# Performance work log

Measured on AMD Instinct MI355X. Metric: run time of the kernel, lower is better.

## Reference

```python
import jax, jax.numpy as jnp
import numpy as np

N = 100000
E = 3200000
NFEAT = 512
NHID = 256


def setup_inputs() -> dict:
    key = jax.random.key(0)
    ks = jax.random.split(key, 8)
    x = jax.random.normal(ks[0], (N, NFEAT), dtype=jnp.float32)
    edge_row = jax.random.randint(ks[1], (E,), 0, N, dtype=jnp.int32)
    edge_col = jax.random.randint(ks[2], (E,), 0, N, dtype=jnp.int32)
    edge_val = jax.random.uniform(ks[3], (E,), dtype=jnp.float32)
    # xavier_uniform init as in reset_parameters
    lim1 = np.sqrt(6.0 / (NFEAT + NHID)).astype(np.float32)
    lim2 = np.sqrt(6.0 / (NHID + NHID)).astype(np.float32)
    W1 = jax.random.uniform(ks[4], (NFEAT, NHID), minval=-lim1, maxval=lim1, dtype=jnp.float32)
    W2 = jax.random.uniform(ks[5], (NHID, NHID), minval=-lim2, maxval=lim2, dtype=jnp.float32)
    b1 = jnp.zeros((NHID,), dtype=jnp.float32)
    b2 = jnp.zeros((NHID,), dtype=jnp.float32)
    alpha = jnp.full((1,), 0.25, dtype=jnp.float32)  # PReLU single weight
    return {"x": x, "edge_row": edge_row, "edge_col": edge_col,
            "edge_val": edge_val, "W1": W1, "b1": b1, "W2": W2, "b2": b2,
            "alpha": alpha}


def _spmm(edge_row, edge_col, edge_val, support):
    # out[i] = sum over edges e with row[e]==i of val[e] * support[col[e]]
    msgs = support[edge_col] * edge_val[:, None]  # [E, F]
    return jax.ops.segment_sum(msgs, edge_row, num_segments=N)


def _prelu(x, alpha):
    return jnp.where(x >= 0, x, alpha * x)


def reference(x, edge_row, edge_col, edge_val, W1, b1, W2, b2, alpha):
    # Layer 1: GraphConvolution(nfeat, nhid) -> PReLU (dropout=0 -> identity)
    h = _spmm(edge_row, edge_col, edge_val, x @ W1) + b1
    h = _prelu(h, alpha)
    # Layer 2: GraphConvolution(nhid, nhid) -> PReLU
    h = _spmm(edge_row, edge_col, edge_val, h @ W2) + b2
    h = _prelu(h, alpha)
    return h
```

## Files before the change

### kernel.cpp

```cpp
#include <hip/hip_runtime.h>

#define NHID 256
#define BSHIFT 6
#define BROWS  (1 << BSHIFT)
#define MAXNB  1568

typedef __attribute__((ext_vector_type(8))) short short8;
typedef __attribute__((ext_vector_type(4))) float floatx4;
typedef __attribute__((ext_vector_type(4))) float float4v;
typedef __attribute__((ext_vector_type(4))) int int4v;
typedef __attribute__((ext_vector_type(4))) unsigned int uint4v;

static __device__ __forceinline__ short f2bf(float f) {
    unsigned u = __float_as_uint(f);
    unsigned r = (u + 0x7fffu + ((u >> 16) & 1u)) >> 16;
    return (short)r;
}
static __device__ __forceinline__ unsigned pk2(float a, float b) {
    return ((unsigned)(unsigned short)f2bf(a)) | (((unsigned)(unsigned short)f2bf(b)) << 16);
}

__global__ void transpose_cast2(const float* __restrict__ W1, short* __restrict__ W1t,
                                const float* __restrict__ W2, short* __restrict__ W2t,
                                int K1, int K2)
{
    int idx = blockIdx.x * 256 + threadIdx.x;
    int n1 = K1 * NHID;
    if (idx < n1) {
        int k = idx >> 8;
        int n = idx & 255;
        W1t[(size_t)n * K1 + k] = f2bf(W1[idx]);
    } else {
        int j = idx - n1;
        if (j < K2 * NHID) {
            int k = j >> 8;
            int n = j & 255;
            W2t[(size_t)n * K2 + k] = f2bf(W2[j]);
        }
    }
}

template<bool ABF16>
__global__ __launch_bounds__(512) void gemm_mfma(
    const void* __restrict__ Ap, const short* __restrict__ Bt,
    short* __restrict__ C, int M, int K)
{
    __shared__ __align__(16) short As[128][40];
    __shared__ __align__(16) short Bs[256][40];

    int tid  = threadIdx.x;
    int m0   = blockIdx.x * 128;
    int lane = tid & 63;
    int wid  = tid >> 6;
    int wm   = wid >> 2;
    int wn   = wid & 3;
    int quad = lane >> 4;
    int l16  = lane & 15;

    floatx4 acc[4][4] = {};

    for (int k0 = 0; k0 < K; k0 += 32) {
        if (ABF16) {
            const short* A = (const short*)Ap;
            int tr = tid >> 2, tc = (tid & 3) * 8;
            int gm = m0 + tr;
            int4v v = {0, 0, 0, 0};
            if (gm < M) v = __builtin_nontemporal_load((const int4v*)(A + (size_t)gm * K + k0 + tc));
            *(int4v*)&As[tr][tc] = v;
        } else {
            const float* A = (const float*)Ap;
            int tr = tid >> 3, tc = (tid & 7) * 4;
            #pragma unroll
            for (int p = 0; p < 2; ++p) {
                int m = p * 64 + tr, gm = m0 + m;
                float4v v = {0.f, 0.f, 0.f, 0.f};
                if (gm < M) v = __builtin_nontemporal_load((const float4v*)(A + (size_t)gm * K + k0 + tc));
                short4 s;
                s.x = f2bf(v.x); s.y = f2bf(v.y); s.z = f2bf(v.z); s.w = f2bf(v.w);
                *(short4*)&As[m][tc] = s;
            }
        }
        {
            int nr = tid >> 2, nc = (tid & 3) * 8;
            #pragma unroll
            for (int p = 0; p < 2; ++p) {
                int n = p * 128 + nr;
                *(int4*)&Bs[n][nc] = *(const int4*)(Bt + (size_t)n * K + k0 + nc);
            }
        }
        __syncthreads();

        short8 af[4], bfr[4];
        #pragma unroll
        for (int t = 0; t < 4; ++t) {
            af[t]  = *(const short8*)&As[wm * 64 + t * 16 + l16][quad * 8];
            bfr[t] = *(const short8*)&Bs[wn * 64 + t * 16 + l16][quad * 8];
        }
        #pragma unroll
        for (int tm = 0; tm < 4; ++tm)
            #pragma unroll
            for (int tn = 0; tn < 4; ++tn)
                acc[tm][tn] = __builtin_amdgcn_mfma_f32_16x16x32_bf16(
                    af[tm], bfr[tn], acc[tm][tn], 0, 0, 0);
        __syncthreads();
    }

    #pragma unroll
    for (int tm = 0; tm < 4; ++tm) {
        #pragma unroll
        for (int r = 0; r < 4; ++r) {
            int row = m0 + wm * 64 + tm * 16 + quad * 4 + r;
            if (row < M) {
                #pragma unroll
                for (int tn = 0; tn < 4; ++tn) {
                    int col = wn * 64 + tn * 16 + l16;
                    C[(size_t)row * NHID + col] = f2bf(acc[tm][tn][r]);
                }
            }
        }
    }
}


__global__ __launch_bounds__(256) void hist_lds(
    const int* __restrict__ erow, int* __restrict__ bcnt, int E, int nb)
{
    __shared__ int h[MAXNB];
    for (int i = threadIdx.x; i < nb; i += 256) h[i] = 0;
    __syncthreads();
    int stride = gridDim.x * 256;
    for (int i = blockIdx.x * 256 + threadIdx.x; i < E; i += stride)
        atomicAdd(&h[erow[i] >> BSHIFT], 1);
    __syncthreads();
    for (int i = threadIdx.x; i < nb; i += 256) {
        int v = h[i];
        if (v) atomicAdd(&bcnt[i], v);
    }
}

__global__ __launch_bounds__(1024) void scan_buckets(
    const int* __restrict__ bcnt, int* __restrict__ bstart,
    int* __restrict__ bcur, int nb, int E)
{
    __shared__ int ws[16];
    __shared__ int carry_s;
    int tid = threadIdx.x, lane = tid & 63, w = tid >> 6;
    if (tid == 0) carry_s = 0;
    __syncthreads();
    for (int base = 0; base < nb; base += 1024) {
        int i = base + tid;
        int v = (i < nb) ? bcnt[i] : 0;
        int x = v;
        #pragma unroll
        for (int off = 1; off < 64; off <<= 1) {
            int y = __shfl_up(x, off, 64);
            if (lane >= off) x += y;
        }
        if (lane == 63) ws[w] = x;
        __syncthreads();
        if (w == 0 && lane < 16) {
            int s2 = ws[lane];
            #pragma unroll
            for (int off = 1; off < 16; off <<= 1) {
                int y = __shfl_up(s2, off, 16);
                if (lane >= off) s2 += y;
            }
            ws[lane] = s2;
        }
        __syncthreads();
        int add = (w > 0) ? ws[w - 1] : 0;
        int incl = x + add;
        int c = carry_s;
        int excl = incl - v + c;
        if (i < nb) { bstart[i] = excl; bcur[i] = excl; }
        __syncthreads();
        if (tid == 1023) carry_s = c + incl;
        __syncthreads();
    }
    if (tid == 0) bstart[nb] = E;
}

__global__ __launch_bounds__(256) void stage_lds(
    const int* __restrict__ erow, const int* __restrict__ ecol,
    const float* __restrict__ eval,
    int* __restrict__ bcur, int2* __restrict__ staged, int E, int nb, int chunk)
{
    __shared__ int h[MAXNB];
    int s = blockIdx.x * chunk;
    int e = min(E, s + chunk);
    for (int i = threadIdx.x; i < nb; i += 256) h[i] = 0;
    __syncthreads();
    for (int i = s + threadIdx.x; i < e; i += 256)
        atomicAdd(&h[erow[i] >> BSHIFT], 1);
    __syncthreads();
    for (int i = threadIdx.x; i < nb; i += 256) {
        int v = h[i];
        h[i] = v ? atomicAdd(&bcur[i], v) : 0;
    }
    __syncthreads();
    for (int i = s + threadIdx.x; i < e; i += 256) {
        int r = erow[i];
        int b = r >> BSHIFT;
        int pos = atomicAdd(&h[b], 1);
        staged[pos] = make_int2(ecol[i] | ((r & (BROWS - 1)) << 20), __float_as_int(eval[i]));
    }
}

__global__ __launch_bounds__(256) void place_rowptr(
    const int* __restrict__ bstart, const int2* __restrict__ staged,
    int2* __restrict__ ep, int* __restrict__ row_ptr, int N, int E)
{
    __shared__ int rcnt[BROWS];
    __shared__ int rbase[BROWS];
    int b  = blockIdx.x;
    int r0 = b << BSHIFT;
    int nr = min(N - r0, BROWS);
    int s = bstart[b], e = bstart[b + 1];
    if (threadIdx.x < BROWS) rcnt[threadIdx.x] = 0;
    __syncthreads();
    for (int i = s + threadIdx.x; i < e; i += 256) {
        int rl = ((unsigned)staged[i].x) >> 20;
        atomicAdd(&rcnt[rl], 1);
    }
    __syncthreads();
    if (threadIdx.x < BROWS) {
        int v = rcnt[threadIdx.x];
        int x = v;
        #pragma unroll
        for (int off = 1; off < 64; off <<= 1) {
            int y = __shfl_up(x, off, 64);
            if (threadIdx.x >= off) x += y;
        }
        int excl = s + x - v;
        rbase[threadIdx.x] = excl;
        if (threadIdx.x < nr) row_ptr[r0 + threadIdx.x] = excl;
        rcnt[threadIdx.x] = 0;
    }
    __syncthreads();
    for (int i = s + threadIdx.x; i < e; i += 256) {
        int2 sv = staged[i];
        int rl = ((unsigned)sv.x) >> 20;
        int slot = rbase[rl] + atomicAdd(&rcnt[rl], 1);
        ep[slot] = make_int2(sv.x & 0xFFFFF, sv.y);
    }
    if (b == gridDim.x - 1 && threadIdx.x == 0) row_ptr[N] = E;
}

static __device__ __forceinline__ void fma8(float* acc, uint4 g, float v)
{
    acc[0] += v * __uint_as_float(g.x << 16);
    acc[1] += v * __uint_as_float(g.x & 0xffff0000u);
    acc[2] += v * __uint_as_float(g.y << 16);
    acc[3] += v * __uint_as_float(g.y & 0xffff0000u);
    acc[4] += v * __uint_as_float(g.z << 16);
    acc[5] += v * __uint_as_float(g.z & 0xffff0000u);
    acc[6] += v * __uint_as_float(g.w << 16);
    acc[7] += v * __uint_as_float(g.w & 0xffff0000u);
}

template<bool OUT_BF16>
__global__ __launch_bounds__(256) void spmm_split(
    const int* __restrict__ row_ptr, const int2* __restrict__ ep,
    const short* __restrict__ dense,
    const float* __restrict__ bias, const float* __restrict__ alpha_p,
    void* __restrict__ outp, int nrows)
{
    int wid  = (blockIdx.x * blockDim.x + threadIdx.x) >> 6;
    int lane = threadIdx.x & 63;
    if (wid >= nrows) return;
    int half = lane >> 5;
    int l32  = lane & 31;
    int s = row_ptr[wid], e = row_ptr[wid + 1];
    int fo = l32 * 8;

    float acc[8] = {};
    int i = s;
    for (; i + 3 < e; i += 4) {
        int2 e0 = ep[i + half];
        int2 e1 = ep[i + 2 + half];
        uint4 g0 = *(const uint4*)(dense + (size_t)e0.x * NHID + fo);
        uint4 g1 = *(const uint4*)(dense + (size_t)e1.x * NHID + fo);
        fma8(acc, g0, __int_as_float(e0.y));
        fma8(acc, g1, __int_as_float(e1.y));
    }
    for (; i < e; i += 2) {
        int j = i + half;
        if (j < e) {
            int2 e0 = ep[j];
            uint4 g0 = *(const uint4*)(dense + (size_t)e0.x * NHID + fo);
            fma8(acc, g0, __int_as_float(e0.y));
        }
    }

    #pragma unroll
    for (int k = 0; k < 8; ++k) acc[k] += __shfl_xor(acc[k], 32, 64);

    float alpha = alpha_p[0];
    float4 b0 = *(const float4*)(bias + fo);
    float4 b1 = *(const float4*)(bias + fo + 4);
    float r[8];
    r[0] = acc[0] + b0.x; r[1] = acc[1] + b0.y; r[2] = acc[2] + b0.z; r[3] = acc[3] + b0.w;
    r[4] = acc[4] + b1.x; r[5] = acc[5] + b1.y; r[6] = acc[6] + b1.z; r[7] = acc[7] + b1.w;
    #pragma unroll
    for (int k = 0; k < 8; ++k) r[k] = (r[k] >= 0.f) ? r[k] : alpha * r[k];

    if (OUT_BF16) {
        if (half == 0) {
            uint4 o;
            o.x = pk2(r[0], r[1]); o.y = pk2(r[2], r[3]);
            o.z = pk2(r[4], r[5]); o.w = pk2(r[6], r[7]);
            *(uint4*)((short*)outp + (size_t)wid * NHID + fo) = o;
        }
    } else {
        float4v ov;
        if (half) { ov.x = r[4]; ov.y = r[5]; ov.z = r[6]; ov.w = r[7]; }
        else      { ov.x = r[0]; ov.y = r[1]; ov.z = r[2]; ov.w = r[3]; }
        __builtin_nontemporal_store(ov, (float4v*)((float*)outp + (size_t)wid * NHID + fo + half * 4));
    }
}

extern "C" void kernel_launch(void* const* d_in, const int* in_sizes, int n_in,
                              void* d_out, int out_size, void* d_ws, size_t ws_size,
                              hipStream_t stream)
{
    const float* x     = (const float*)d_in[0];
    const int*   erow  = (const int*)d_in[1];
    const int*   ecol  = (const int*)d_in[2];
    const float* eval  = (const float*)d_in[3];
    const float* W1    = (const float*)d_in[4];
    const float* b1    = (const float*)d_in[5];
    const float* W2    = (const float*)d_in[6];
    const float* b2    = (const float*)d_in[7];
    const float* alpha = (const float*)d_in[8];

    int NFEAT = 512;
    int N = in_sizes[0] / NFEAT;
    int E = in_sizes[1];
    float* out = (float*)d_out;

    char* wsp = (char*)d_ws;
    short* support_b = (short*)wsp;  wsp += (size_t)N * NHID * sizeof(short);
    short* h1b       = (short*)wsp;  wsp += (size_t)N * NHID * sizeof(short);
    int2*  ep        = (int2*)wsp;   wsp += (size_t)E * sizeof(int2);
    int*   row_ptr   = (int*)wsp;    wsp += ((size_t)(N + 1) * sizeof(int) + 15) & ~(size_t)15;
    short* W1t       = (short*)wsp;  wsp += (size_t)NFEAT * NHID * sizeof(short);
    short* W2t       = (short*)wsp;  wsp += (size_t)NHID * NHID * sizeof(short);

    int NB = (N + BROWS - 1) >> BSHIFT;

    int* bcnt   = (int*)h1b;
    int* bstart = bcnt + NB;
    int* bcur   = bstart + NB + 1;

    int2* staged = (int2*)support_b;

    transpose_cast2<<<((NFEAT + NHID) * NHID + 255) / 256, 256, 0, stream>>>(
        W1, W1t, W2, W2t, NFEAT, NHID);

    hipMemsetAsync(bcnt, 0, (size_t)NB * sizeof(int), stream);
    int nwg = 256;
    int chunk = (E + nwg - 1) / nwg;
    hist_lds<<<nwg, 256, 0, stream>>>(erow, bcnt, E, NB);
    scan_buckets<<<1, 1024, 0, stream>>>(bcnt, bstart, bcur, NB, E);
    stage_lds<<<nwg, 256, 0, stream>>>(erow, ecol, eval, bcur, staged, E, NB, chunk);
    place_rowptr<<<NB, 256, 0, stream>>>(bstart, staged, ep, row_ptr, N, E);

    int ggrid = (N + 127) / 128;
    int spmm_blocks = (N + 3) / 4;

    gemm_mfma<false><<<ggrid, 512, 0, stream>>>(x, W1t, support_b, N, NFEAT);
    spmm_split<true><<<spmm_blocks, 256, 0, stream>>>(row_ptr, ep, support_b, b1, alpha, h1b, N);
    gemm_mfma<true><<<ggrid, 512, 0, stream>>>(h1b, W2t, support_b, N, NHID);
    spmm_split<false><<<spmm_blocks, 256, 0, stream>>>(row_ptr, ep, support_b, b2, alpha, out, N);
}
```

Measured before the change: 988.4 us.

## Split SpMM feature columns into 8 slices with 16 edges per wave

Rewrites the SpMM so each row is processed by 8 blocks, each covering a 32-column slice. Within a wave, 16 lane-groups handle different edges in parallel and 4 lanes cover the slice, followed by a butterfly shuffle reduction. The goal is more memory-level parallelism per row, since with about 32 edges per row nearly all of them can be fetched at once instead of the previous 2 at a time. The cost is 8x more blocks, ep and row_ptr being re-read by every slice, 64-byte gather segments instead of full 512-byte rows, and extra shuffle reductions.

Result: slower. 1.345 ms (+36.0%).

```diff
diff --git a/kernel.cpp b/kernel.cpp
--- a/kernel.cpp
+++ b/kernel.cpp
@@ -259,63 +259,64 @@
 }
 
 template<bool OUT_BF16>
-__global__ __launch_bounds__(256) void spmm_split(
+__global__ __launch_bounds__(256) void spmm_slice(
     const int* __restrict__ row_ptr, const int2* __restrict__ ep,
     const short* __restrict__ dense,
     const float* __restrict__ bias, const float* __restrict__ alpha_p,
     void* __restrict__ outp, int nrows)
 {
-    int wid  = (blockIdx.x * blockDim.x + threadIdx.x) >> 6;
+    int sl  = blockIdx.x & 7;
+    int rg  = blockIdx.x >> 3;
+    int wv  = threadIdx.x >> 6;
+    int row = rg * 4 + wv;
+    if (row >= nrows) return;
     int lane = threadIdx.x & 63;
-    if (wid >= nrows) return;
-    int half = lane >> 5;
-    int l32  = lane & 31;
-    int s = row_ptr[wid], e = row_ptr[wid + 1];
-    int fo = l32 * 8;
+    int g = lane >> 2;
+    int q = lane & 3;
+    int co = sl * 32 + q * 8;
+    int es = row_ptr[row], ee = row_ptr[row + 1];
 
     float acc[8] = {};
-    int i = s;
-    for (; i + 3 < e; i += 4) {
-        int2 e0 = ep[i + half];
-        int2 e1 = ep[i + 2 + half];
-        uint4 g0 = *(const uint4*)(dense + (size_t)e0.x * NHID + fo);
-        uint4 g1 = *(const uint4*)(dense + (size_t)e1.x * NHID + fo);
-        fma8(acc, g0, __int_as_float(e0.y));
-        fma8(acc, g1, __int_as_float(e1.y));
-    }
-    for (; i < e; i += 2) {
-        int j = i + half;
-        if (j < e) {
+    for (int i = es; i < ee; i += 16) {
+        int j = i + g;
+        if (j < ee) {
             int2 e0 = ep[j];
-            uint4 g0 = *(const uint4*)(dense + (size_t)e0.x * NHID + fo);
-            fma8(acc, g0, __int_as_float(e0.y));
+            uint4 gv = *(const uint4*)(dense + (size_t)e0.x * NHID + co);
+            fma8(acc, gv, __int_as_float(e0.y));
         }
     }
 
     #pragma unroll
-    for (int k = 0; k < 8; ++k) acc[k] += __shfl_xor(acc[k], 32, 64);
-
-    float alpha = alpha_p[0];
-    float4 b0 = *(const float4*)(bias + fo);
-    float4 b1 = *(const float4*)(bias + fo + 4);
-    float r[8];
-    r[0] = acc[0] + b0.x; r[1] = acc[1] + b0.y; r[2] = acc[2] + b0.z; r[3] = acc[3] + b0.w;
-    r[4] = acc[4] + b1.x; r[5] = acc[5] + b1.y; r[6] = acc[6] + b1.z; r[7] = acc[7] + b1.w;
-    #pragma unroll
-    for (int k = 0; k < 8; ++k) r[k] = (r[k] >= 0.f) ? r[k] : alpha * r[k];
-
-    if (OUT_BF16) {
-        if (half == 0) {
+    for (int k = 0; k < 8; ++k) {
+        acc[k] += __shfl_xor(acc[k], 4, 64);
+        acc[k] += __shfl_xor(acc[k], 8, 64);
+        acc[k] += __shfl_xor(acc[k], 16, 64);
+        acc[k] += __shfl_xor(acc[k], 32, 64);
+    }
+
+    if (g == 0) {
+        float alpha = alpha_p[0];
+        float4 b0 = *(const float4*)(bias + co);
+        float4 b1 = *(const float4*)(bias + co + 4);
+        float r[8];
+        r[0] = acc[0] + b0.x; r[1] = acc[1] + b0.y; r[2] = acc[2] + b0.z; r[3] = acc[3] + b0.w;
+        r[4] = acc[4] + b1.x; r[5] = acc[5] + b1.y; r[6] = acc[6] + b1.z; r[7] = acc[7] + b1.w;
+        #pragma unroll
+        for (int k = 0; k < 8; ++k) r[k] = (r[k] >= 0.f) ? r[k] : alpha * r[k];
+
+        if (OUT_BF16) {
             uint4 o;
             o.x = pk2(r[0], r[1]); o.y = pk2(r[2], r[3]);
             o.z = pk2(r[4], r[5]); o.w = pk2(r[6], r[7]);
-            *(uint4*)((short*)outp + (size_t)wid * NHID + fo) = o;
-        }
-    } else {
-        float4v ov;
-        if (half) { ov.x = r[4]; ov.y = r[5]; ov.z = r[6]; ov.w = r[7]; }
-        else      { ov.x = r[0]; ov.y = r[1]; ov.z = r[2]; ov.w = r[3]; }
-        __builtin_nontemporal_store(ov, (float4v*)((float*)outp + (size_t)wid * NHID + fo + half * 4));
+            *(uint4*)((short*)outp + (size_t)row * NHID + co) = o;
+        } else {
+            float4v o0, o1;
+            o0.x = r[0]; o0.y = r[1]; o0.z = r[2]; o0.w = r[3];
+            o1.x = r[4]; o1.y = r[5]; o1.z = r[6]; o1.w = r[7];
+            float* op = (float*)outp + (size_t)row * NHID + co;
+            __builtin_nontemporal_store(o0, (float4v*)op);
+            __builtin_nontemporal_store(o1, (float4v*)(op + 4));
+        }
     }
 }
 
@@ -366,10 +367,10 @@
     place_rowptr<<<NB, 256, 0, stream>>>(bstart, staged, ep, row_ptr, N, E);
 
     int ggrid = (N + 127) / 128;
-    int spmm_blocks = (N + 3) / 4;
+    int spmm_grid = ((N + 3) / 4) * 8;
 
     gemm_mfma<false><<<ggrid, 512, 0, stream>>>(x, W1t, support_b, N, NFEAT);
-    spmm_split<true><<<spmm_blocks, 256, 0, stream>>>(row_ptr, ep, support_b, b1, alpha, h1b, N);
+    spmm_slice<true><<<spmm_grid, 256, 0, stream>>>(row_ptr, ep, support_b, b1, alpha, h1b, N);
     gemm_mfma<true><<<ggrid, 512, 0, stream>>>(h1b, W2t, support_b, N, NHID);
-    spmm_split<false><<<spmm_blocks, 256, 0, stream>>>(row_ptr, ep, support_b, b2, alpha, out, N);
-}
+    spmm_slice<false><<<spmm_grid, 256, 0, stream>>>(row_ptr, ep, support_b, b2, alpha, out, N);
+}
```
